# Performance work log

Hardware: AMD Instinct MI355X
Metric: run time of the kernel (lower is better)

Reference implementation:

```python
import jax, jax.numpy as jnp
import numpy as np

C_CURV = 1.0          # Poincare ball curvature
EPS = 1e-5
MAX_NORM = (1.0 - 1e-4) / np.sqrt(C_CURV)


def _artanh(x):
    x = jnp.clip(x, -1.0 + 1e-5, 1.0 - 1e-5)
    return 0.5 * (jnp.log1p(x) - jnp.log1p(-x))


def _expmap0(v):
    # v: [N,C,H,W]; norm over channel dim per spatial location
    n = jnp.maximum(jnp.linalg.norm(v, axis=1, keepdims=True), EPS)
    sc = np.sqrt(C_CURV)
    return jnp.tanh(sc * n) * v / (sc * n)


def _logmap0(y):
    n = jnp.maximum(jnp.linalg.norm(y, axis=1, keepdims=True), EPS)
    sc = np.sqrt(C_CURV)
    return _artanh(sc * n) * y / (sc * n)


def _project(y):
    # clamp back inside the ball
    n = jnp.maximum(jnp.linalg.norm(y, axis=1, keepdims=True), EPS)
    return jnp.where(n > MAX_NORM, y * (MAX_NORM / n), y)


def _conv3x3(u, w, b):
    y = jax.lax.conv_general_dilated(u, w, window_strides=(1, 1),
                                     padding=((1, 1), (1, 1)),
                                     dimension_numbers=('NCHW', 'OIHW', 'NCHW'))
    return y + b[None, :, None, None]


def _hconv(x, w, b):
    # HConvolution2d: tangent-space conv around origin
    return _project(_expmap0(_conv3x3(_logmap0(x), w, b)))


def _hbn(x, gamma, beta):
    # HBatchNorm2d: Euclidean BN in the tangent space at the origin (training stats)
    u = _logmap0(x)
    m = u.mean(axis=(0, 2, 3), keepdims=True)
    v = u.var(axis=(0, 2, 3), keepdims=True)
    u = (u - m) / jnp.sqrt(v + 1e-5)
    u = u * gamma[None, :, None, None] + beta[None, :, None, None]
    return _project(_expmap0(u))


def _hrelu(x):
    return _project(_expmap0(jax.nn.relu(_logmap0(x))))


def setup_inputs() -> dict:
    key = jax.random.key(0)
    ks = jax.random.split(key, 8)
    N, Cin, Cmid, Cout, H, W = 8, 32, 32, 32, 256, 256
    # input point on the Poincare ball
    x = _project(_expmap0(0.1 * jax.random.normal(ks[0], (N, Cin, H, W), jnp.float32)))
    fan1 = Cin * 9
    fan2 = Cmid * 9
    w1 = jax.random.normal(ks[1], (Cmid, Cin, 3, 3), jnp.float32) / np.sqrt(fan1)
    b1 = jnp.zeros((Cmid,), jnp.float32)
    g1 = jnp.ones((Cmid,), jnp.float32)
    beta1 = jnp.zeros((Cmid,), jnp.float32)
    w2 = jax.random.normal(ks[2], (Cout, Cmid, 3, 3), jnp.float32) / np.sqrt(fan2)
    b2 = jnp.zeros((Cout,), jnp.float32)
    g2 = jnp.ones((Cout,), jnp.float32)
    beta2 = jnp.zeros((Cout,), jnp.float32)
    return {"x": x, "w1": w1, "b1": b1, "g1": g1, "beta1": beta1,
            "w2": w2, "b2": b2, "g2": g2, "beta2": beta2}


def reference(x, w1, b1, g1, beta1, w2, b2, g2, beta2):
    out = _hconv(x, w1, b1)
    out = _hbn(out, g1, beta1)
    out = _hrelu(out)
    out = _hconv(out, w2, b2)
    out = _hbn(out, g2, beta2)
    out = _hrelu(out)
    return out
```

## Files before the change

kernel.cpp:

```cpp
#include <hip/hip_runtime.h>
#include <math.h>

#define HWDIM 256
#define CH 32
#define NB 8
#define TILE 16
#define NLOC (NB*HWDIM*HWDIM)
#define R_CLAMP 4.9517189f
#define MAXN 0.9999f
#define BN_EPS 1e-5f
#define EPSF 1e-5f
#define NBLK 2048
#define OST 264

typedef __attribute__((ext_vector_type(8))) _Float16 half8;
typedef __attribute__((ext_vector_type(4))) _Float16 half4;
typedef __attribute__((ext_vector_type(4))) float floatx4;

__device__ __forceinline__ float artanh_c(float n) {
    float t = fminf(n, 1.0f - 1e-5f);
    return 0.5f * (log1pf(t) - log1pf(-t));
}

__global__ __launch_bounds__(256) void wprep_kernel(
    const float* __restrict__ w1, const float* __restrict__ w2,
    _Float16* __restrict__ wp1, _Float16* __restrict__ wp2)
{
    int idx = blockIdx.x * 256 + threadIdx.x;
    if (idx >= 2*CH*CH*9) return;
    int s = idx >= CH*CH*9;
    int id = idx - s*(CH*CH*9);
    const float* w = s ? w2 : w1;
    _Float16* wp = s ? wp2 : wp1;
    int j  = id & 7;
    int r  = id >> 3;
    int co = r & 31;
    int og = r >> 5;
    int g  = og & 3;
    int o  = og >> 2;
    int ci = g*8 + j;
    wp[id] = (_Float16)w[(co*CH + ci)*9 + o];
}

template<int STAGE>
__global__ __launch_bounds__(256) void conv_mfma_kernel(
    const void* __restrict__ srcv,
    const _Float16* __restrict__ wp,
    const float* __restrict__ bias,
    const float* __restrict__ scsh,
    _Float16* __restrict__ dst,
    float* __restrict__ partials)
{
    __shared__ _Float16 ah[10368];
    __shared__ float red[4][64];

    const int tid = threadIdx.x;
    const int flat = blockIdx.x;
    const int bz = flat & 7;
    const int t  = flat >> 3;
    const int by = t >> 4, bx = t & 15;
    const int h0 = by*TILE - 1, w0 = bx*TILE - 1;

    for (int loc = tid; loc < 324; loc += 256) {
        int y = loc / 18, x = loc - y*18;
        int gh = h0 + y, gw = w0 + x;
        if (gh < 0 || gh >= HWDIM || gw < 0 || gw >= HWDIM) {
            half8 z = {0,0,0,0,0,0,0,0};
            #pragma unroll
            for (int g = 0; g < 4; g++) *(half8*)(ah + ((y*4+g)*18 + x)*8) = z;
            continue;
        }
        float v[CH]; float n2 = 0.f;
        if (STAGE == 1) {
            const float* p = (const float*)srcv + ((size_t)bz*CH << 16) + gh*HWDIM + gw;
            #pragma unroll
            for (int c = 0; c < CH; c++) { float t0 = p[(size_t)c << 16]; v[c] = t0; n2 = fmaf(t0, t0, n2); }
            float n = fmaxf(sqrtf(n2), EPSF);
            float f = artanh_c(n) / n;
            #pragma unroll
            for (int c = 0; c < CH; c++) v[c] *= f;
        } else {
            const _Float16* p = (const _Float16*)srcv + (((size_t)bz << 16) + gh*HWDIM + gw)*CH;
            half8 raw[4];
            #pragma unroll
            for (int k = 0; k < 4; k++) raw[k] = *(const half8*)(p + 8*k);
            #pragma unroll
            for (int c = 0; c < CH; c++) {
                float t0 = fmaf((float)raw[c>>3][c&7], scsh[c], scsh[CH + c]);
                v[c] = t0; n2 = fmaf(t0, t0, n2);
            }
            float n = sqrtf(n2);
            float f = (n > R_CLAMP) ? (R_CLAMP / n) : 1.0f;
            #pragma unroll
            for (int c = 0; c < CH; c++) v[c] = fmaxf(v[c]*f, 0.0f);
        }
        #pragma unroll
        for (int g = 0; g < 4; g++) {
            half8 hv;
            #pragma unroll
            for (int j = 0; j < 8; j++) hv[j] = (_Float16)v[g*8 + j];
            *(half8*)(ah + ((y*4+g)*18 + x)*8) = hv;
        }
    }
    __syncthreads();

    const int lane = tid & 63, wave = tid >> 6;
    const int xx = lane & 15, q = lane >> 4;

    floatx4 acc[4][2];
    #pragma unroll
    for (int i = 0; i < 4; i++) {
        acc[i][0] = (floatx4){0.f,0.f,0.f,0.f};
        acc[i][1] = (floatx4){0.f,0.f,0.f,0.f};
    }

    #pragma unroll
    for (int dx = 0; dx < 3; dx++) {
        half8 af[6];
        #pragma unroll
        for (int yy = 0; yy < 6; yy++)
            af[yy] = *(const half8*)(ah + (((wave*4+yy)*4 + q)*18 + xx + dx)*8);
        #pragma unroll
        for (int dy = 0; dy < 3; dy++) {
            const int o = dy*3 + dx;
            const _Float16* wb = wp + (size_t)((o*4 + q)*32)*8;
            half8 wf0 = *(const half8*)(wb + xx*8);
            half8 wf1 = *(const half8*)(wb + (xx+16)*8);
            #pragma unroll
            for (int i = 0; i < 4; i++) {
                acc[i][0] = __builtin_amdgcn_mfma_f32_16x16x32_f16(wf0, af[i+dy], acc[i][0], 0,0,0);
                acc[i][1] = __builtin_amdgcn_mfma_f32_16x16x32_f16(wf1, af[i+dy], acc[i][1], 0,0,0);
            }
        }
    }

    float bs[8];
    #pragma unroll
    for (int r = 0; r < 4; r++) { bs[r] = bias[q*4+r]; bs[4+r] = bias[q*4+r+16]; }
    float sv[8], qv[8];
    #pragma unroll
    for (int k = 0; k < 8; k++) { sv[k] = 0.f; qv[k] = 0.f; }

    _Float16* dp = dst + (((size_t)bz << 16) + (size_t)(by*TILE)*HWDIM + bx*TILE + xx)*CH + q*4;

    #pragma unroll
    for (int i = 0; i < 4; i++) {
        float n2 = 0.f;
        #pragma unroll
        for (int r = 0; r < 4; r++) {
            acc[i][0][r] += bs[r];
            acc[i][1][r] += bs[4+r];
            n2 = fmaf(acc[i][0][r], acc[i][0][r], n2);
            n2 = fmaf(acc[i][1][r], acc[i][1][r], n2);
        }
        n2 += __shfl_xor(n2, 16, 64);
        n2 += __shfl_xor(n2, 32, 64);
        float nn = sqrtf(n2);
        float f = (nn > R_CLAMP) ? (R_CLAMP/nn) : 1.0f;
        half4 o0, o1;
        #pragma unroll
        for (int r = 0; r < 4; r++) {
            float a0 = acc[i][0][r] * f;
            float a1 = acc[i][1][r] * f;
            sv[r]   += a0; qv[r]   = fmaf(a0, a0, qv[r]);
            sv[4+r] += a1; qv[4+r] = fmaf(a1, a1, qv[4+r]);
            o0[r] = (_Float16)a0; o1[r] = (_Float16)a1;
        }
        _Float16* a = dp + (size_t)(wave*4 + i)*HWDIM*CH;
        *(half4*)(a)      = o0;
        *(half4*)(a + 16) = o1;
    }

    #pragma unroll
    for (int k = 0; k < 8; k++) {
        #pragma unroll
        for (int m = 1; m < 16; m <<= 1) {
            sv[k] += __shfl_xor(sv[k], m, 64);
            qv[k] += __shfl_xor(qv[k], m, 64);
        }
    }
    if (xx == 0) {
        #pragma unroll
        for (int r = 0; r < 4; r++) {
            red[wave][q*4+r]        = sv[r];
            red[wave][16 + q*4+r]   = sv[4+r];
            red[wave][32 + q*4+r]   = qv[r];
            red[wave][48 + q*4+r]   = qv[4+r];
        }
    }
    __syncthreads();
    if (tid < 64) {
        float s = red[0][tid] + red[1][tid] + red[2][tid] + red[3][tid];
        partials[(size_t)tid*NBLK + flat] = s;
    }
}

__global__ __launch_bounds__(256) void finalize_kernel(
    const float* __restrict__ partials,
    const float* __restrict__ g, const float* __restrict__ beta,
    float* __restrict__ scsh)
{
    __shared__ float ss[256], sq[256];
    const int c = blockIdx.x;
    const int tid = threadIdx.x;
    float s = 0.f, q = 0.f;
    for (int b = tid; b < NBLK; b += 256) {
        s += partials[(size_t)c*NBLK + b];
        q += partials[(size_t)(CH + c)*NBLK + b];
    }
    ss[tid] = s; sq[tid] = q;
    __syncthreads();
    for (int st = 128; st > 0; st >>= 1) {
        if (tid < st) { ss[tid] += ss[tid+st]; sq[tid] += sq[tid+st]; }
        __syncthreads();
    }
    if (tid == 0) {
        const float NS = (float)NLOC;
        float mean = ss[0] / NS;
        float var = fmaxf(sq[0] / NS - mean*mean, 0.0f);
        float sc = g[c] / sqrtf(var + BN_EPS);
        scsh[c] = sc;
        scsh[CH + c] = beta[c] - mean*sc;
    }
}

__global__ __launch_bounds__(256) void out_kernel(
    const _Float16* __restrict__ t4c, const float* __restrict__ scsh,
    float* __restrict__ out)
{
    __shared__ float outb[16*OST];
    const int w = threadIdx.x;
    const int h = blockIdx.x, n = blockIdx.y;
    const _Float16* p = t4c + (((size_t)n << 16) + (size_t)h*HWDIM + w)*CH;
    half8 raw[4];
    #pragma unroll
    for (int k = 0; k < 4; k++) raw[k] = *(const half8*)(p + 8*k);
    float u[CH]; float n2 = 0.f;
    #pragma unroll
    for (int c = 0; c < CH; c++) {
        float t = fmaf((float)raw[c>>3][c&7], scsh[c], scsh[CH+c]);
        u[c] = t; n2 = fmaf(t, t, n2);
    }
    float nn = sqrtf(n2);
    float f = (nn > R_CLAMP) ? (R_CLAMP/nn) : 1.0f;
    float r2 = 0.f;
    #pragma unroll
    for (int c = 0; c < CH; c++) { float r = fmaxf(u[c]*f, 0.0f); u[c] = r; r2 = fmaf(r, r, r2); }
    float rn = fmaxf(sqrtf(r2), EPSF);
    float s = fminf(tanhf(rn), MAXN) / rn;
    #pragma unroll
    for (int c = 0; c < CH; c++) u[c] *= s;

    #pragma unroll
    for (int hf = 0; hf < 2; hf++) {
        if (hf) __syncthreads();
        #pragma unroll
        for (int c = 0; c < 16; c++) outb[c*OST + w] = u[hf*16 + c];
        __syncthreads();
        int co = threadIdx.x >> 4, seg = threadIdx.x & 15;
        const float* row = outb + co*OST + seg*16;
        float* gp = out + ((size_t)(n*CH + hf*16 + co) << 16) + (size_t)h*HWDIM + seg*16;
        #pragma unroll
        for (int k = 0; k < 4; k++) *(floatx4*)(gp + 4*k) = *(const floatx4*)(row + 4*k);
    }
}

extern "C" void kernel_launch(void* const* d_in, const int* in_sizes, int n_in,
                              void* d_out, int out_size, void* d_ws, size_t ws_size,
                              hipStream_t stream)
{
    const float* x   = (const float*)d_in[0];
    const float* w1  = (const float*)d_in[1];
    const float* b1  = (const float*)d_in[2];
    const float* g1  = (const float*)d_in[3];
    const float* be1 = (const float*)d_in[4];
    const float* w2  = (const float*)d_in[5];
    const float* b2  = (const float*)d_in[6];
    const float* g2  = (const float*)d_in[7];
    const float* be2 = (const float*)d_in[8];
    float* outf = (float*)d_out;

    char* ws = (char*)d_ws;
    _Float16* wp1   = (_Float16*)ws;
    _Float16* wp2   = wp1 + 9216;
    float* partials = (float*)(ws + 36864);
    float* scsh1    = (float*)(ws + 36864 + 524288);
    float* scsh2    = scsh1 + 64;
    _Float16* t1c   = (_Float16*)(scsh2 + 64);
    _Float16* t4c   = t1c + (size_t)NLOC*CH;

    wprep_kernel<<<72, 256, 0, stream>>>(w1, w2, wp1, wp2);

    conv_mfma_kernel<1><<<NBLK, 256, 0, stream>>>(x, wp1, b1, scsh1, t1c, partials);
    finalize_kernel<<<32, 256, 0, stream>>>(partials, g1, be1, scsh1);
    conv_mfma_kernel<2><<<NBLK, 256, 0, stream>>>(t1c, wp2, b2, scsh1, t4c, partials);
    finalize_kernel<<<32, 256, 0, stream>>>(partials, g2, be2, scsh2);
    out_kernel<<<dim3(HWDIM, NB), 256, 0, stream>>>(t4c, scsh2, outf);
}
```

Measured before the change: 203.5 us.

## Split logmap into pre-pass, process two tiles per block with prefetch, fast math

A new pre_kernel does the stage-1 logmap and writes fp16 channel-last data, so the first conv reads contiguous half8 vectors instead of strided fp32 channel loads. Each conv block now covers two adjacent 16x16 tiles and prefetches the next tile's halo while the MFMA loop runs. The change also adds s_setprio around the MFMAs, launch_bounds occupancy hints, and fast intrinsics (__logf, __expf, __fdividef) for artanh, tanh and the divisions. The cost is an extra full-tensor fp16 write and read, one more launch, and somewhat lower precision in the transcendental functions.

```diff
diff --git a/kernel.cpp b/kernel.cpp
--- a/kernel.cpp
+++ b/kernel.cpp
@@ -10,16 +10,17 @@
 #define MAXN 0.9999f
 #define BN_EPS 1e-5f
 #define EPSF 1e-5f
-#define NBLK 2048
+#define TPB 2
+#define GRIDC 1024
 #define OST 264
 
 typedef __attribute__((ext_vector_type(8))) _Float16 half8;
 typedef __attribute__((ext_vector_type(4))) _Float16 half4;
 typedef __attribute__((ext_vector_type(4))) float floatx4;
 
-__device__ __forceinline__ float artanh_c(float n) {
+__device__ __forceinline__ float artanh_fast(float n) {
     float t = fminf(n, 1.0f - 1e-5f);
-    return 0.5f * (log1pf(t) - log1pf(-t));
+    return 0.5f * __logf(__fdividef(1.0f + t, 1.0f - t));
 }
 
 __global__ __launch_bounds__(256) void wprep_kernel(
@@ -42,9 +43,62 @@
     wp[id] = (_Float16)w[(co*CH + ci)*9 + o];
 }
 
+__global__ __launch_bounds__(256) void pre_kernel(
+    const float* __restrict__ x, _Float16* __restrict__ t0c)
+{
+    const int w = threadIdx.x;
+    const int h = blockIdx.x, n = blockIdx.y;
+    const float* p = x + ((size_t)(n*CH) << 16) + (size_t)h*HWDIM + w;
+    float v[CH]; float n2 = 0.f;
+    #pragma unroll
+    for (int c = 0; c < CH; c++) { float t = p[(size_t)c << 16]; v[c] = t; n2 = fmaf(t, t, n2); }
+    float nn = fmaxf(sqrtf(n2), EPSF);
+    float f = __fdividef(artanh_fast(nn), nn);
+    _Float16* dp = t0c + (((size_t)n << 16) + (size_t)h*HWDIM + w)*CH;
+    #pragma unroll
+    for (int g = 0; g < 4; g++) {
+        half8 hv;
+        #pragma unroll
+        for (int j = 0; j < 8; j++) hv[j] = (_Float16)(v[g*8 + j] * f);
+        *(half8*)(dp + g*8) = hv;
+    }
+}
+
 template<int STAGE>
-__global__ __launch_bounds__(256) void conv_mfma_kernel(
-    const void* __restrict__ srcv,
+__device__ __forceinline__ void xform_store(const half8* pr, bool inb,
+                                            _Float16* base, const float* __restrict__ scsh)
+{
+    if (!inb) {
+        half8 z = {0,0,0,0,0,0,0,0};
+        #pragma unroll
+        for (int g = 0; g < 4; g++) *(half8*)(base + g*144) = z;
+        return;
+    }
+    if (STAGE == 1) {
+        #pragma unroll
+        for (int g = 0; g < 4; g++) *(half8*)(base + g*144) = pr[g];
+    } else {
+        float v[CH]; float n2 = 0.f;
+        #pragma unroll
+        for (int c = 0; c < CH; c++) {
+            float t0 = fmaf((float)pr[c>>3][c&7], scsh[c], scsh[CH + c]);
+            v[c] = t0; n2 = fmaf(t0, t0, n2);
+        }
+        float n = sqrtf(n2);
+        float f = (n > R_CLAMP) ? __fdividef(R_CLAMP, n) : 1.0f;
+        #pragma unroll
+        for (int g = 0; g < 4; g++) {
+            half8 hv;
+            #pragma unroll
+            for (int j = 0; j < 8; j++) hv[j] = (_Float16)fmaxf(v[g*8 + j]*f, 0.0f);
+            *(half8*)(base + g*144) = hv;
+        }
+    }
+}
+
+template<int STAGE>
+__global__ __launch_bounds__(256, 4) void conv_mfma_kernel(
+    const _Float16* __restrict__ src,
     const _Float16* __restrict__ wp,
     const float* __restrict__ bias,
     const float* __restrict__ scsh,
@@ -55,84 +109,39 @@
     __shared__ float red[4][64];
 
     const int tid = threadIdx.x;
-    const int flat = blockIdx.x;
-    const int bz = flat & 7;
-    const int t  = flat >> 3;
-    const int by = t >> 4, bx = t & 15;
-    const int h0 = by*TILE - 1, w0 = bx*TILE - 1;
-
-    for (int loc = tid; loc < 324; loc += 256) {
-        int y = loc / 18, x = loc - y*18;
-        int gh = h0 + y, gw = w0 + x;
-        if (gh < 0 || gh >= HWDIM || gw < 0 || gw >= HWDIM) {
-            half8 z = {0,0,0,0,0,0,0,0};
-            #pragma unroll
-            for (int g = 0; g < 4; g++) *(half8*)(ah + ((y*4+g)*18 + x)*8) = z;
-            continue;
-        }
-        float v[CH]; float n2 = 0.f;
-        if (STAGE == 1) {
-            const float* p = (const float*)srcv + ((size_t)bz*CH << 16) + gh*HWDIM + gw;
-            #pragma unroll
-            for (int c = 0; c < CH; c++) { float t0 = p[(size_t)c << 16]; v[c] = t0; n2 = fmaf(t0, t0, n2); }
-            float n = fmaxf(sqrtf(n2), EPSF);
-            float f = artanh_c(n) / n;
-            #pragma unroll
-            for (int c = 0; c < CH; c++) v[c] *= f;
-        } else {
-            const _Float16* p = (const _Float16*)srcv + (((size_t)bz << 16) + gh*HWDIM + gw)*CH;
-            half8 raw[4];
-            #pragma unroll
-            for (int k = 0; k < 4; k++) raw[k] = *(const half8*)(p + 8*k);
-            #pragma unroll
-            for (int c = 0; c < CH; c++) {
-                float t0 = fmaf((float)raw[c>>3][c&7], scsh[c], scsh[CH + c]);
-                v[c] = t0; n2 = fmaf(t0, t0, n2);
-            }
-            float n = sqrtf(n2);
-            float f = (n > R_CLAMP) ? (R_CLAMP / n) : 1.0f;
-            #pragma unroll
-            for (int c = 0; c < CH; c++) v[c] = fmaxf(v[c]*f, 0.0f);
-        }
-        #pragma unroll
-        for (int g = 0; g < 4; g++) {
-            half8 hv;
-            #pragma unroll
-            for (int j = 0; j < 8; j++) hv[j] = (_Float16)v[g*8 + j];
-            *(half8*)(ah + ((y*4+g)*18 + x)*8) = hv;
-        }
-    }
-    __syncthreads();
+    const int b   = blockIdx.x;
+    const int bz  = b & 7;
+    const int tb  = b >> 3;
+    const int by  = tb >> 3;
+    const int bx0 = (tb & 7) * TPB;
+    const int h0  = by*TILE - 1;
+    const int wbase = bx0*TILE - 1;
+
+    const int sy0 = tid / 18, sx0 = tid - sy0*18;
+    const int gh0 = h0 + sy0;
+    const bool row0 = (gh0 >= 0) & (gh0 < HWDIM);
+    const bool has1 = tid < 68;
+    const int l1 = tid + 256;
+    const int sy1 = l1 / 18, sx1 = l1 - sy1*18;
+    const int gh1 = h0 + sy1;
+    const bool row1 = has1 & (gh1 >= 0) & (gh1 < HWDIM);
+    _Float16* const base0 = ah + ((sy0*4)*18 + sx0)*8;
+    _Float16* const base1 = ah + ((sy1*4)*18 + sx1)*8;
 
     const int lane = tid & 63, wave = tid >> 6;
     const int xx = lane & 15, q = lane >> 4;
 
-    floatx4 acc[4][2];
-    #pragma unroll
-    for (int i = 0; i < 4; i++) {
-        acc[i][0] = (floatx4){0.f,0.f,0.f,0.f};
-        acc[i][1] = (floatx4){0.f,0.f,0.f,0.f};
-    }
-
-    #pragma unroll
-    for (int dx = 0; dx < 3; dx++) {
-        half8 af[6];
-        #pragma unroll
-        for (int yy = 0; yy < 6; yy++)
-            af[yy] = *(const half8*)(ah + (((wave*4+yy)*4 + q)*18 + xx + dx)*8);
-        #pragma unroll
-        for (int dy = 0; dy < 3; dy++) {
-            const int o = dy*3 + dx;
-            const _Float16* wb = wp + (size_t)((o*4 + q)*32)*8;
-            half8 wf0 = *(const half8*)(wb + xx*8);
-            half8 wf1 = *(const half8*)(wb + (xx+16)*8);
-            #pragma unroll
-            for (int i = 0; i < 4; i++) {
-                acc[i][0] = __builtin_amdgcn_mfma_f32_16x16x32_f16(wf0, af[i+dy], acc[i][0], 0,0,0);
-                acc[i][1] = __builtin_amdgcn_mfma_f32_16x16x32_f16(wf1, af[i+dy], acc[i][1], 0,0,0);
-            }
-        }
-    }
+    half8 p0[4];
+    bool in0 = false;
+
+    #define PREF(jj) do {                                                              \
+        int gw0 = wbase + (jj)*TILE + sx0;                                             \
+        in0 = row0 & (gw0 >= 0) & (gw0 < HWDIM);                                       \
+        if (in0) {                                                                     \
+            const half8* p = (const half8*)(src + (((size_t)bz << 16) + gh0*HWDIM + gw0)*CH); \
+            p0[0]=p[0]; p0[1]=p[1]; p0[2]=p[2]; p0[3]=p[3];                            \
+        }                                                                              \
+    } while (0)
 
     float bs[8];
     #pragma unroll
@@ -141,34 +150,82 @@
     #pragma unroll
     for (int k = 0; k < 8; k++) { sv[k] = 0.f; qv[k] = 0.f; }
 
-    _Float16* dp = dst + (((size_t)bz << 16) + (size_t)(by*TILE)*HWDIM + bx*TILE + xx)*CH + q*4;
-
-    #pragma unroll
-    for (int i = 0; i < 4; i++) {
-        float n2 = 0.f;
-        #pragma unroll
-        for (int r = 0; r < 4; r++) {
-            acc[i][0][r] += bs[r];
-            acc[i][1][r] += bs[4+r];
-            n2 = fmaf(acc[i][0][r], acc[i][0][r], n2);
-            n2 = fmaf(acc[i][1][r], acc[i][1][r], n2);
-        }
-        n2 += __shfl_xor(n2, 16, 64);
-        n2 += __shfl_xor(n2, 32, 64);
-        float nn = sqrtf(n2);
-        float f = (nn > R_CLAMP) ? (R_CLAMP/nn) : 1.0f;
-        half4 o0, o1;
-        #pragma unroll
-        for (int r = 0; r < 4; r++) {
-            float a0 = acc[i][0][r] * f;
-            float a1 = acc[i][1][r] * f;
-            sv[r]   += a0; qv[r]   = fmaf(a0, a0, qv[r]);
-            sv[4+r] += a1; qv[4+r] = fmaf(a1, a1, qv[4+r]);
-            o0[r] = (_Float16)a0; o1[r] = (_Float16)a1;
-        }
-        _Float16* a = dp + (size_t)(wave*4 + i)*HWDIM*CH;
-        *(half4*)(a)      = o0;
-        *(half4*)(a + 16) = o1;
+    PREF(0);
+
+    #pragma unroll 1
+    for (int j = 0; j < TPB; j++) {
+        half8 t1r[4]; bool tin1 = false;
+        if (has1) {
+            int gw1 = wbase + j*TILE + sx1;
+            tin1 = row1 & (gw1 >= 0) & (gw1 < HWDIM);
+            if (tin1) {
+                const half8* p = (const half8*)(src + (((size_t)bz << 16) + gh1*HWDIM + gw1)*CH);
+                t1r[0]=p[0]; t1r[1]=p[1]; t1r[2]=p[2]; t1r[3]=p[3];
+            }
+        }
+        xform_store<STAGE>(p0, in0, base0, scsh);
+        if (has1) xform_store<STAGE>(t1r, tin1, base1, scsh);
+        __syncthreads();
+        if (j + 1 < TPB) PREF(j + 1);
+
+        floatx4 acc[4][2];
+        #pragma unroll
+        for (int i = 0; i < 4; i++) {
+            acc[i][0] = (floatx4){0.f,0.f,0.f,0.f};
+            acc[i][1] = (floatx4){0.f,0.f,0.f,0.f};
+        }
+
+        __builtin_amdgcn_s_setprio(1);
+        #pragma unroll
+        for (int dx = 0; dx < 3; dx++) {
+            half8 af[6];
+            #pragma unroll
+            for (int yy = 0; yy < 6; yy++)
+                af[yy] = *(const half8*)(ah + (((wave*4+yy)*4 + q)*18 + xx + dx)*8);
+            #pragma unroll
+            for (int dy = 0; dy < 3; dy++) {
+                const int o = dy*3 + dx;
+                const _Float16* wb = wp + (size_t)((o*4 + q)*32)*8;
+                half8 wf0 = *(const half8*)(wb + xx*8);
+                half8 wf1 = *(const half8*)(wb + (xx+16)*8);
+                #pragma unroll
+                for (int i = 0; i < 4; i++) {
+                    acc[i][0] = __builtin_amdgcn_mfma_f32_16x16x32_f16(wf0, af[i+dy], acc[i][0], 0,0,0);
+                    acc[i][1] = __builtin_amdgcn_mfma_f32_16x16x32_f16(wf1, af[i+dy], acc[i][1], 0,0,0);
+                }
+            }
+        }
+        __builtin_amdgcn_s_setprio(0);
+
+        _Float16* dp = dst + (((size_t)bz << 16) + (size_t)(by*TILE)*HWDIM + (bx0 + j)*TILE + xx)*CH + q*4;
+        #pragma unroll
+        for (int i = 0; i < 4; i++) {
+            float n2 = 0.f;
+            #pragma unroll
+            for (int r = 0; r < 4; r++) {
+                acc[i][0][r] += bs[r];
+                acc[i][1][r] += bs[4+r];
+                n2 = fmaf(acc[i][0][r], acc[i][0][r], n2);
+                n2 = fmaf(acc[i][1][r], acc[i][1][r], n2);
+            }
+            n2 += __shfl_xor(n2, 16, 64);
+            n2 += __shfl_xor(n2, 32, 64);
+            float nn = sqrtf(n2);
+            float f = (nn > R_CLAMP) ? __fdividef(R_CLAMP, nn) : 1.0f;
+            half4 o0, o1;
+            #pragma unroll
+            for (int r = 0; r < 4; r++) {
+                float a0 = acc[i][0][r] * f;
+                float a1 = acc[i][1][r] * f;
+                sv[r]   += a0; qv[r]   = fmaf(a0, a0, qv[r]);
+                sv[4+r] += a1; qv[4+r] = fmaf(a1, a1, qv[4+r]);
+                o0[r] = (_Float16)a0; o1[r] = (_Float16)a1;
+            }
+            _Float16* a = dp + (size_t)(wave*4 + i)*HWDIM*CH;
+            *(half4*)(a)      = o0;
+            *(half4*)(a + 16) = o1;
+        }
+        __syncthreads();
     }
 
     #pragma unroll
@@ -191,8 +248,9 @@
     __syncthreads();
     if (tid < 64) {
         float s = red[0][tid] + red[1][tid] + red[2][tid] + red[3][tid];
-        partials[(size_t)tid*NBLK + flat] = s;
-    }
+        partials[(size_t)tid*GRIDC + b] = s;
+    }
+    #undef PREF
 }
 
 __global__ __launch_bounds__(256) void finalize_kernel(
@@ -204,9 +262,9 @@
     const int c = blockIdx.x;
     const int tid = threadIdx.x;
     float s = 0.f, q = 0.f;
-    for (int b = tid; b < NBLK; b += 256) {
-        s += partials[(size_t)c*NBLK + b];
-        q += partials[(size_t)(CH + c)*NBLK + b];
+    for (int b = tid; b < GRIDC; b += 256) {
+        s += partials[(size_t)c*GRIDC + b];
+        q += partials[(size_t)(CH + c)*GRIDC + b];
     }
     ss[tid] = s; sq[tid] = q;
     __syncthreads();
@@ -242,12 +300,14 @@
         u[c] = t; n2 = fmaf(t, t, n2);
     }
     float nn = sqrtf(n2);
-    float f = (nn > R_CLAMP) ? (R_CLAMP/nn) : 1.0f;
+    float f = (nn > R_CLAMP) ? __fdividef(R_CLAMP, nn) : 1.0f;
     float r2 = 0.f;
     #pragma unroll
     for (int c = 0; c < CH; c++) { float r = fmaxf(u[c]*f, 0.0f); u[c] = r; r2 = fmaf(r, r, r2); }
     float rn = fmaxf(sqrtf(r2), EPSF);
-    float s = fminf(tanhf(rn), MAXN) / rn;
+    float a = __expf(2.0f * rn);
+    float th = __fdividef(a - 1.0f, a + 1.0f);
+    float s = __fdividef(fminf(th, MAXN), rn);
     #pragma unroll
     for (int c = 0; c < CH; c++) u[c] *= s;
 
@@ -284,16 +344,17 @@
     _Float16* wp1   = (_Float16*)ws;
     _Float16* wp2   = wp1 + 9216;
     float* partials = (float*)(ws + 36864);
-    float* scsh1    = (float*)(ws + 36864 + 524288);
+    float* scsh1    = (float*)(ws + 36864 + 262144);
     float* scsh2    = scsh1 + 64;
-    _Float16* t1c   = (_Float16*)(scsh2 + 64);
-    _Float16* t4c   = t1c + (size_t)NLOC*CH;
+    _Float16* bufA  = (_Float16*)(scsh2 + 64);
+    _Float16* bufB  = bufA + (size_t)NLOC*CH;
 
     wprep_kernel<<<72, 256, 0, stream>>>(w1, w2, wp1, wp2);
-
-    conv_mfma_kernel<1><<<NBLK, 256, 0, stream>>>(x, wp1, b1, scsh1, t1c, partials);
+    pre_kernel<<<dim3(HWDIM, NB), 256, 0, stream>>>(x, bufA);
+
+    conv_mfma_kernel<1><<<GRIDC, 256, 0, stream>>>(bufA, wp1, b1, scsh1, bufB, partials);
     finalize_kernel<<<32, 256, 0, stream>>>(partials, g1, be1, scsh1);
-    conv_mfma_kernel<2><<<NBLK, 256, 0, stream>>>(t1c, wp2, b2, scsh1, t4c, partials);
+    conv_mfma_kernel<2><<<GRIDC, 256, 0, stream>>>(bufB, wp2, b2, scsh1, bufA, partials);
     finalize_kernel<<<32, 256, 0, stream>>>(partials, g2, be2, scsh2);
-    out_kernel<<<dim3(HWDIM, NB), 256, 0, stream>>>(t4c, scsh2, outf);
-}
+    out_kernel<<<dim3(HWDIM, NB), 256, 0, stream>>>(bufA, scsh2, outf);
+}
```

Result: slower. 290.0 us (+42.5%).
